# Performance work log

Hardware: AMD Instinct MI355X
Metric: run time of the kernel (lower is better)

## Reference

```python
import jax, jax.numpy as jnp
import numpy as np


def conv2d(x, w):
    # kernel_mult2d: VALID cross-correlation, NCHW/OIHW
    return jax.lax.conv_general_dilated(x, w, (1, 1), 'VALID',
                                        dimension_numbers=('NCHW', 'OIHW', 'NCHW'))


def setup_inputs() -> dict:
    key = jax.random.key(0)
    kx, kw = jax.random.split(key)
    B, C, H, W = 32, 16, 64, 64
    O, K = 256, 5
    x = jax.random.normal(kx, (B, C, H, W), dtype=jnp.float32)
    stdv = 1.0 / np.sqrt(C * K * K)  # nn.init.uniform_(-stdv, stdv)
    weight = jax.random.uniform(kw, (O, C, K, K), dtype=jnp.float32,
                                minval=-stdv, maxval=stdv)
    return {"x": x, "weight": weight}


def reference(x, weight):
    O, C, kh, kw = weight.shape
    # forward output: y = out_act(out_sim(x, weight)) with identity activation
    y = conv2d(x, weight)                                   # [B, O, Ho, Wo]

    # ---- compute_update (training branch, alpha != 0) ----
    # lrn_sim == out_sim, lrn_act == identity -> s == y
    s = y.transpose(0, 2, 3, 1).reshape(-1, O)              # [N, O], N = B*Ho*Wo
    N = s.shape[0]

    # unfold_map2d: patches with channel-major layout (C outer, kh*kw inner),
    # then permute(0,2,3,1,4).view(N, -1) -> [N, C*kh*kw]
    patches = jax.lax.conv_general_dilated_patches(
        x, (kh, kw), (1, 1), 'VALID',
        dimension_numbers=('NCHW', 'OIHW', 'NCHW'))         # [B, C*kh*kw, Ho, Wo]
    x_unf = patches.transpose(0, 2, 3, 1).reshape(N, -1)    # [N, D], D = C*kh*kw

    # competitive winner-take-all (no random abstention)
    winner_mask = (s == s.max(axis=1, keepdims=True)).astype(s.dtype)

    # lfb off; lfb_value == 0.0 so lfb_out == winner_mask; hebb rule: r = lfb_out * y
    r = winner_mask * s                                     # [N, O]

    # reconstruction 'qnt': x_bar = w; reduction 'mean':
    # delta_w[o, d] = mean_n r[n, o] * (x_unf[n, d] - w[o, d])
    # factor the outer-product mean to avoid the [N, O, D] intermediate
    w_flat = weight.reshape(O, -1)                          # [O, D]
    delta_w = (r.T @ x_unf) / N - r.mean(axis=0)[:, None] * w_flat

    return y, delta_w.reshape(weight.shape)
```

## Files before the change

kernel.cpp:

```cpp
#include <hip/hip_runtime.h>
#include <hip/hip_bf16.h>

#define B_  32
#define C_  16
#define Hh  64
#define Ww  64
#define O_  256
#define Kk  5
#define Ho_ 60
#define Wo_ 60
#define Dd  400
#define Nn  (B_*Ho_*Wo_)
#define NY  ((size_t)B_*O_*Ho_*Wo_)
#define OVCAP 1024
#define TAU 2.5e-4f
#define NSL 16
#define NCHK 60

typedef float f4 __attribute__((ext_vector_type(4)));
typedef float f32x16 __attribute__((ext_vector_type(16)));
typedef unsigned int u32x2 __attribute__((ext_vector_type(2)));
typedef unsigned int u32x4 __attribute__((ext_vector_type(4)));
typedef __bf16 bf16x8 __attribute__((ext_vector_type(8)));

static __device__ __forceinline__ void bf16split(float v, unsigned short& h, unsigned short& l) {
    __hip_bfloat16 bh = __float2bfloat16(v);
    float vh = __bfloat162float(bh);
    __hip_bfloat16 bl = __float2bfloat16(v - vh);
    h = __builtin_bit_cast(unsigned short, bh);
    l = __builtin_bit_cast(unsigned short, bl);
}

__global__ void prep_kernel(const float* __restrict__ w, unsigned short* __restrict__ wpkH,
                            unsigned short* __restrict__ wpkL, int* __restrict__ ovcnt,
                            int* __restrict__ done, float* __restrict__ dout) {
    const int u = blockIdx.x;
    const int jc = u / 5, s5 = u - (u / 5) * 5;
    const int tid = threadIdx.x;
    const int ot = tid >> 5, r32 = tid & 31;
    const int o = 32 * ot + r32;
    #pragma unroll
    for (int q2 = 0; q2 < 2; ++q2) {
        unsigned short h[8], l[8];
        #pragma unroll
        for (int j = 0; j < 8; ++j) {
            int g = 16 * s5 + 8 * q2 + j;
            bf16split(w[o * Dd + g * 5 + jc], h[j], l[j]);
        }
        const size_t off = ((size_t)(u * 8 + ot) * 64 + (r32 + 32 * q2)) * 8;
        u32x4 ph = { (unsigned)h[0] | ((unsigned)h[1] << 16), (unsigned)h[2] | ((unsigned)h[3] << 16),
                     (unsigned)h[4] | ((unsigned)h[5] << 16), (unsigned)h[6] | ((unsigned)h[7] << 16) };
        u32x4 pl = { (unsigned)l[0] | ((unsigned)l[1] << 16), (unsigned)l[2] | ((unsigned)l[3] << 16),
                     (unsigned)l[4] | ((unsigned)l[5] << 16), (unsigned)l[6] | ((unsigned)l[7] << 16) };
        *reinterpret_cast<u32x4*>(wpkH + off) = ph;
        *reinterpret_cast<u32x4*>(wpkL + off) = pl;
    }
    {
        float* dz = dout + NY + ((size_t)u * 256 + tid) * 16;
        f4 z = { 0.f, 0.f, 0.f, 0.f };
        *reinterpret_cast<f4*>(dz)      = z;
        *reinterpret_cast<f4*>(dz + 4)  = z;
        *reinterpret_cast<f4*>(dz + 8)  = z;
        *reinterpret_cast<f4*>(dz + 12) = z;
    }
    if (u == 0 && tid == 0) { *ovcnt = 0; *done = 0; }
}

__launch_bounds__(256, 3)
__global__ void conv_mfma_kernel(const float* __restrict__ x, const float* __restrict__ w,
                                 const unsigned short* __restrict__ wpkH,
                                 const unsigned short* __restrict__ wpkL, float* __restrict__ y,
                                 unsigned short* __restrict__ winner, float* __restrict__ wsv,
                                 int* __restrict__ ovn, int* __restrict__ ovo,
                                 float* __restrict__ ovs, int* __restrict__ ovcnt) {
    __shared__ __align__(16) unsigned short xT[2 * 7072];
    __shared__ float wm1[4][64], wm2[4][64];
    __shared__ float rowM1[64];
    __shared__ float rowMv[64];
    __shared__ int   rowO[64];
    __shared__ float xrow[Dd];
    __shared__ float red[256];
    __shared__ int   ambl[16];
    __shared__ int   ambc, nm;

    const int tid = threadIdx.x;
    const int L = tid & 63, wv = tid >> 6;
    const int q2 = L >> 5, r32 = L & 31;
    const int bid = (int)((blockIdx.x & 7) * 240 + (blockIdx.x >> 3));
    const int b = bid / Ho_, ho = bid % Ho_;

    if (tid == 0) ambc = 0;

    const unsigned short* ah0 = wpkH + (size_t)(2 * wv) * 512 + (size_t)L * 8;
    const unsigned short* al0 = wpkL + (size_t)(2 * wv) * 512 + (size_t)L * 8;

    u32x4 AH_[3][2], AL_[3][2];
    #pragma unroll
    for (int ot = 0; ot < 2; ++ot) {
        AH_[0][ot] = *reinterpret_cast<const u32x4*>(ah0 + ot * 512);
        AL_[0][ot] = *reinterpret_cast<const u32x4*>(al0 + ot * 512);
        AH_[1][ot] = *reinterpret_cast<const u32x4*>(ah0 + 4096 + ot * 512);
        AL_[1][ot] = *reinterpret_cast<const u32x4*>(al0 + 4096 + ot * 512);
    }

    if (tid < 80) {
        u32x4 z = { 0, 0, 0, 0 };
        int plane = tid / 40, rem = tid % 40, row = 64 + rem / 10, blk = rem % 10;
        *reinterpret_cast<u32x4*>(&xT[plane * 7072 + row * 104 + blk * 8]) = z;
    }

    {
        const float* xb = x + (size_t)b * (C_ * Hh * Ww);
        const int v = tid & 63;
        const int seg = tid >> 6;
        const int segc = seg * 4;
        #pragma unroll
        for (int qg = 0; qg < 5; ++qg) {
            unsigned short h[4], l[4];
            #pragma unroll
            for (int gg = 0; gg < 4; ++gg) {
                const int k = qg * 4 + gg;
                const int kc = k / 5, ki = k % 5;
                float val = xb[((segc + kc) * Hh + ho + ki) * Ww + v];
                bf16split(val, h[gg], l[gg]);
            }
            const int g0 = seg * 20 + qg * 4;
            u32x2 ph = { (unsigned)h[0] | ((unsigned)h[1] << 16),
                         (unsigned)h[2] | ((unsigned)h[3] << 16) };
            u32x2 pl = { (unsigned)l[0] | ((unsigned)l[1] << 16),
                         (unsigned)l[2] | ((unsigned)l[3] << 16) };
            *reinterpret_cast<u32x2*>(&xT[v * 104 + g0]) = ph;
            *reinterpret_cast<u32x2*>(&xT[7072 + v * 104 + g0]) = pl;
        }
    }

    f32x16 acc[2][2];
    #pragma unroll
    for (int ot = 0; ot < 2; ++ot)
        #pragma unroll
        for (int wt = 0; wt < 2; ++wt)
            #pragma unroll
            for (int i = 0; i < 16; ++i) acc[ot][wt][i] = 0.f;

    __syncthreads();

    u32x4 BH_[2][2], BL_[2][2];
    #pragma unroll
    for (int wt = 0; wt < 2; ++wt) {
        const int bbase = (32 * wt + r32 + 0) * 104 + 0 + 8 * q2;
        BH_[0][wt] = *reinterpret_cast<const u32x4*>(&xT[bbase]);
        BL_[0][wt] = *reinterpret_cast<const u32x4*>(&xT[7072 + bbase]);
    }

    #pragma unroll
    for (int u = 0; u < 25; ++u) {
        const int cur = u % 3;
        const int curB = u & 1, nxtB = curB ^ 1;
        if (u < 23) {
            const int nxtA = (u + 2) % 3;
            #pragma unroll
            for (int ot = 0; ot < 2; ++ot) {
                AH_[nxtA][ot] = *reinterpret_cast<const u32x4*>(ah0 + (u + 2) * 4096 + ot * 512);
                AL_[nxtA][ot] = *reinterpret_cast<const u32x4*>(al0 + (u + 2) * 4096 + ot * 512);
            }
        }
        if (u < 24) {
            const int jcn = (u + 1) / 5, s5n = (u + 1) % 5;
            #pragma unroll
            for (int wt = 0; wt < 2; ++wt) {
                const int bbase = (32 * wt + r32 + jcn) * 104 + 16 * s5n + 8 * q2;
                BH_[nxtB][wt] = *reinterpret_cast<const u32x4*>(&xT[bbase]);
                BL_[nxtB][wt] = *reinterpret_cast<const u32x4*>(&xT[7072 + bbase]);
            }
        }
        __builtin_amdgcn_sched_barrier(0);
        #pragma unroll
        for (int p = 0; p < 3; ++p) {
            #pragma unroll
            for (int ot = 0; ot < 2; ++ot) {
                #pragma unroll
                for (int wt = 0; wt < 2; ++wt) {
                    bf16x8 Aop = __builtin_bit_cast(bf16x8, (p == 2) ? AL_[cur][ot] : AH_[cur][ot]);
                    bf16x8 Bop = __builtin_bit_cast(bf16x8, (p == 1) ? BL_[curB][wt] : BH_[curB][wt]);
                    acc[ot][wt] = __builtin_amdgcn_mfma_f32_32x32x16_bf16(Aop, Bop, acc[ot][wt], 0, 0, 0);
                }
            }
        }
    }

    #pragma unroll
    for (int wt = 0; wt < 2; ++wt) {
        float m1 = -__builtin_inff(), m2 = -__builtin_inff();
        #pragma unroll
        for (int ot = 0; ot < 2; ++ot)
            #pragma unroll
            for (int i = 0; i < 16; ++i) {
                float v = acc[ot][wt][i];
                m2 = fmaxf(m2, fminf(m1, v));
                m1 = fmaxf(m1, v);
            }
        float o1 = __shfl_xor(m1, 32), o2 = __shfl_xor(m2, 32);
        m2 = fmaxf(fminf(m1, o1), fmaxf(m2, o2));
        m1 = fmaxf(m1, o1);
        if (q2 == 0) { wm1[wv][32 * wt + r32] = m1; wm2[wv][32 * wt + r32] = m2; }
    }
    __syncthreads();
    if (tid < 64) {
        const int p = tid;
        float M1 = wm1[0][p], M2 = wm2[0][p];
        #pragma unroll
        for (int w2 = 1; w2 < 4; ++w2) {
            float c1 = wm1[w2][p], c2 = wm2[w2][p];
            M2 = fmaxf(fminf(M1, c1), fmaxf(M2, c2));
            M1 = fmaxf(M1, c1);
        }
        bool amb = (M1 - M2) < TAU;
        if (amb && p < Wo_) {
            int pos = atomicAdd(&ambc, 1);
            if (pos < 16) ambl[pos] = p;
        }
        rowM1[p] = amb ? __builtin_inff() : M1;
        rowMv[p] = M1;
        rowO[p] = 0;
    }
    __syncthreads();

    #pragma unroll
    for (int wt = 0; wt < 2; ++wt) {
        const int wo = 32 * wt + r32;
        if (wo < Wo_) {
            const float M = rowM1[wo];
            #pragma unroll
            for (int ot = 0; ot < 2; ++ot)
                #pragma unroll
                for (int i = 0; i < 16; ++i) {
                    if (acc[ot][wt][i] == M)
                        rowO[wo] = 64 * wv + 32 * ot + (i & 3) + 8 * (i >> 2) + 4 * q2;
                }
        }
    }
    __syncthreads();
    if (tid < Wo_) {
        const int n = (b * Ho_ + ho) * Wo_ + tid;
        winner[n] = (unsigned short)rowO[tid];
        wsv[n] = rowMv[tid];
    }

    #pragma unroll
    for (int ot = 0; ot < 2; ++ot)
        #pragma unroll
        for (int wt = 0; wt < 2; ++wt) {
            const int wo = 32 * wt + r32;
            if (wo < Wo_) {
                #pragma unroll
                for (int i = 0; i < 16; ++i) {
                    const int o = 64 * wv + 32 * ot + (i & 3) + 8 * (i >> 2) + 4 * q2;
                    __builtin_nontemporal_store(acc[ot][wt][i],
                        y + ((size_t)(b * O_ + o) * Ho_ + ho) * (size_t)Wo_ + wo);
                }
            }
        }

    __syncthreads();
    const int na = (ambc < 16) ? ambc : 16;
    for (int a = 0; a < na; ++a) {
        const int wo = ambl[a];
        const int n = (b * Ho_ + ho) * Wo_ + wo;
        for (int k = tid; k < Dd; k += 256) {
            int c = k / 25, rr = k % 25, i = rr / 5, j = rr % 5;
            xrow[k] = x[(((size_t)b * C_ + c) * Hh + (ho + i)) * Ww + (wo + j)];
        }
        if (tid == 0) nm = 0;
        __syncthreads();
        const int o = tid;
        const float* wr = w + (size_t)o * Dd;
        float s = 0.f;
        #pragma unroll 4
        for (int k = 0; k < Dd; ++k) s = fmaf(xrow[k], wr[k], s);
        red[o] = s;
        __syncthreads();
        #pragma unroll
        for (int st = 128; st >= 1; st >>= 1) {
            if (o < st) red[o] = fmaxf(red[o], red[o + st]);
            __syncthreads();
        }
        const float mx = red[0];
        if (s == mx) {
            int k2 = atomicAdd(&nm, 1);
            if (k2 == 0) { winner[n] = (unsigned short)o; wsv[n] = mx; }
            else {
                int q = atomicAdd(ovcnt, 1);
                if (q < OVCAP) { ovn[q] = n; ovo[q] = o; ovs[q] = mx; }
            }
        }
        __syncthreads();
    }
}

__global__ void sort_kernel(const unsigned short* __restrict__ winner, const float* __restrict__ wsv,
                            int* __restrict__ h, int* __restrict__ done,
                            const int* __restrict__ ovn, const int* __restrict__ ovo,
                            const float* __restrict__ ovs, const int* __restrict__ ovcnt,
                            int* __restrict__ lw_n, float* __restrict__ lw_s,
                            int* __restrict__ count, int cap) {
    __shared__ int lh[O_];
    __shared__ int cur[O_];
    const int blk = blockIdx.x, tid = threadIdx.x;
    lh[tid] = 0;
    __syncthreads();
    const int n0 = blk * (Nn / NCHK);
    for (int i = tid; i < Nn / NCHK; i += 256)
        atomicAdd(&lh[(int)winner[n0 + i]], 1);
    __syncthreads();
    h[blk * O_ + tid] = lh[tid];
    __threadfence();
    __syncthreads();
    if (tid == 0) {
        atomicAdd(done, 1);
        while (atomicAdd(done, 0) < NCHK) __builtin_amdgcn_s_sleep(8);
        __threadfence();
    }
    __syncthreads();
    int basev = 0;
    for (int bb = 0; bb < blk; ++bb) basev += h[bb * O_ + tid];
    cur[tid] = basev;
    if (blk == 0) {
        int tot = 0;
        for (int bb = 0; bb < NCHK; ++bb) tot += h[bb * O_ + tid];
        int oc = *ovcnt; if (oc > OVCAP) oc = OVCAP;
        int cnt = tot;
        for (int e = 0; e < oc; ++e) {
            if (ovo[e] == tid && cnt < cap) {
                lw_n[(size_t)tid * cap + cnt] = ovn[e];
                lw_s[(size_t)tid * cap + cnt] = ovs[e];
                ++cnt;
            }
        }
        count[tid] = (cnt < cap) ? cnt : cap;
    }
    __syncthreads();
    for (int i = tid; i < Nn / NCHK; i += 256) {
        const int n = n0 + i;
        const int o = (int)winner[n];
        int pos = atomicAdd(&cur[o], 1);
        if (pos < cap) {
            lw_n[(size_t)o * cap + pos] = n;
            lw_s[(size_t)o * cap + pos] = wsv[n];
        }
    }
}

__global__ void delta_part_kernel(const float* __restrict__ x, const float* __restrict__ w,
                                  const int* __restrict__ count, const int* __restrict__ lw_n,
                                  const float* __restrict__ lw_s, float* __restrict__ dout,
                                  int cap) {
    const int o   = blockIdx.x / NSL;
    const int sl  = blockIdx.x % NSL;
    const int tid = threadIdx.x;
    int cnt = count[o]; if (cnt > cap) cnt = cap;
    const int e0 = (int)(((long long)cnt * sl) / NSL);
    const int e1 = (int)(((long long)cnt * (sl + 1)) / NSL);

    const int d0 = tid;
    const int c0 = d0 / 25, r0 = d0 % 25, i0 = r0 / 5, j0 = r0 % 5;
    const bool has1 = (tid < Dd - 256);
    const int dd1 = has1 ? tid + 256 : 0;
    const int c1 = dd1 / 25, r1 = dd1 % 25, i1 = r1 / 5, j1 = r1 % 5;
    const int off0 = c0 * (Hh * Ww) + i0 * Ww + j0;
    const int off1 = c1 * (Hh * Ww) + i1 * Ww + j1;

    const int* ln = lw_n + (size_t)o * cap;
    const float* ls = lw_s + (size_t)o * cap;

    float acc0 = 0.f, acc1 = 0.f, ssum = 0.f;
    int nA = 0, nB = 0; float sA = 0.f, sB = 0.f;
    if (e0 < e1)     { nA = ln[e0];     sA = ls[e0]; }
    if (e0 + 1 < e1) { nB = ln[e0 + 1]; sB = ls[e0 + 1]; }
    float xA0 = 0.f, xA1 = 0.f;
    if (e0 < e1) {
        int bb = nA / 3600, rem = nA - bb * 3600, hh = rem / 60, ww2 = rem - hh * 60;
        const float* xb = x + (size_t)bb * (C_ * Hh * Ww) + hh * Ww + ww2;
        xA0 = xb[off0]; if (has1) xA1 = xb[off1];
    }
    for (int e = e0; e < e1; ++e) {
        float xB0 = 0.f, xB1 = 0.f;
        if (e + 1 < e1) {
            int bb = nB / 3600, rem = nB - bb * 3600, hh = rem / 60, ww2 = rem - hh * 60;
            const float* xb = x + (size_t)bb * (C_ * Hh * Ww) + hh * Ww + ww2;
            xB0 = xb[off0]; if (has1) xB1 = xb[off1];
        }
        int nC = 0; float sC = 0.f;
        if (e + 2 < e1) { nC = ln[e + 2]; sC = ls[e + 2]; }
        ssum += sA; acc0 += sA * xA0; acc1 += sA * xA1;
        nA = nB; sA = sB; xA0 = xB0; xA1 = xB1;
        nB = nC; sB = sC;
    }
    if (e0 < e1) {
        const float invN = 1.0f / (float)Nn;
        atomicAdd(dout + NY + (size_t)o * Dd + d0, acc0 * invN - ssum * invN * w[o * Dd + d0]);
        if (has1)
            atomicAdd(dout + NY + (size_t)o * Dd + dd1, acc1 * invN - ssum * invN * w[o * Dd + dd1]);
    }
}

extern "C" void kernel_launch(void* const* d_in, const int* in_sizes, int n_in,
                              void* d_out, int out_size, void* d_ws, size_t ws_size,
                              hipStream_t stream) {
    (void)in_sizes; (void)n_in; (void)out_size;
    const float* x = (const float*)d_in[0];
    const float* w = (const float*)d_in[1];
    float* out = (float*)d_out;

    char* ws = (char*)d_ws;
    int*            count  = (int*)ws;
    int*            ovcnt  = (int*)(ws + 1024);
    int*            done   = (int*)(ws + 1088);
    unsigned short* wpkH   = (unsigned short*)(ws + 1152);
    unsigned short* wpkL   = (unsigned short*)(ws + 205952);
    unsigned short* winner = (unsigned short*)(ws + 410752);
    float*          wsv    = (float*)(ws + 641152);
    int*            ovn    = (int*)(ws + 1101952);
    int*            ovo    = (int*)(ws + 1106048);
    float*          ovs    = (float*)(ws + 1110144);
    int*            hist   = (int*)(ws + 1114240);
    const size_t base = 1175680;

    size_t avail = (ws_size > base) ? (ws_size - base) : 0;
    long long cap_ll = (long long)(avail / ((size_t)O_ * 8));
    int cap = (int)(cap_ll > 4096 ? 4096 : (cap_ll < 1 ? 1 : cap_ll));

    int*   lw_n = (int*)(ws + base);
    float* lw_s = (float*)(ws + base + (size_t)O_ * cap * 4);

    prep_kernel<<<dim3(25), dim3(256), 0, stream>>>(w, wpkH, wpkL, ovcnt, done, out);
    conv_mfma_kernel<<<dim3(B_ * Ho_), dim3(256), 0, stream>>>(x, w, wpkH, wpkL, out, winner, wsv,
                                                               ovn, ovo, ovs, ovcnt);
    sort_kernel<<<dim3(NCHK), dim3(256), 0, stream>>>(winner, wsv, hist, done,
                                                      ovn, ovo, ovs, ovcnt,
                                                      lw_n, lw_s, count, cap);
    delta_part_kernel<<<dim3(O_ * NSL), dim3(256), 0, stream>>>(x, w, count, lw_n, lw_s, out, cap);
}
```

Before: 191.0 us.

## Move ambiguous-winner exact recompute out of conv kernel into separate fallback kernel

The conv kernel no longer recomputes ambiguous winner positions in fp32 inline. It appends them to a global list, and a new grid-strided fallback kernel processes that list afterwards. This takes the serialized per-block recompute loop and its shared buffers out of the conv kernel, which lowers LDS use and removes tail imbalance between blocks. The cost is an extra kernel launch, global atomics on a single counter, and a fixed capacity for ambiguous entries.

```diff
diff --git a/kernel.cpp b/kernel.cpp
--- a/kernel.cpp
+++ b/kernel.cpp
@@ -12,6 +12,7 @@
 #define Dd  400
 #define Nn  (B_*Ho_*Wo_)
 #define NY  ((size_t)B_*O_*Ho_*Wo_)
+#define ACAP 16384
 #define OVCAP 1024
 #define TAU 2.5e-4f
 #define NSL 16
@@ -32,8 +33,9 @@
 }
 
 __global__ void prep_kernel(const float* __restrict__ w, unsigned short* __restrict__ wpkH,
-                            unsigned short* __restrict__ wpkL, int* __restrict__ ovcnt,
-                            int* __restrict__ done, float* __restrict__ dout) {
+                            unsigned short* __restrict__ wpkL, int* __restrict__ acnt,
+                            int* __restrict__ ovcnt, int* __restrict__ done,
+                            float* __restrict__ dout) {
     const int u = blockIdx.x;
     const int jc = u / 5, s5 = u - (u / 5) * 5;
     const int tid = threadIdx.x;
@@ -63,33 +65,25 @@
         *reinterpret_cast<f4*>(dz + 8)  = z;
         *reinterpret_cast<f4*>(dz + 12) = z;
     }
-    if (u == 0 && tid == 0) { *ovcnt = 0; *done = 0; }
+    if (u == 0 && tid == 0) { *acnt = 0; *ovcnt = 0; *done = 0; }
 }
 
 __launch_bounds__(256, 3)
-__global__ void conv_mfma_kernel(const float* __restrict__ x, const float* __restrict__ w,
-                                 const unsigned short* __restrict__ wpkH,
+__global__ void conv_mfma_kernel(const float* __restrict__ x, const unsigned short* __restrict__ wpkH,
                                  const unsigned short* __restrict__ wpkL, float* __restrict__ y,
                                  unsigned short* __restrict__ winner, float* __restrict__ wsv,
-                                 int* __restrict__ ovn, int* __restrict__ ovo,
-                                 float* __restrict__ ovs, int* __restrict__ ovcnt) {
+                                 int* __restrict__ acnt, int* __restrict__ ambig) {
     __shared__ __align__(16) unsigned short xT[2 * 7072];
     __shared__ float wm1[4][64], wm2[4][64];
     __shared__ float rowM1[64];
     __shared__ float rowMv[64];
     __shared__ int   rowO[64];
-    __shared__ float xrow[Dd];
-    __shared__ float red[256];
-    __shared__ int   ambl[16];
-    __shared__ int   ambc, nm;
 
     const int tid = threadIdx.x;
     const int L = tid & 63, wv = tid >> 6;
     const int q2 = L >> 5, r32 = L & 31;
     const int bid = (int)((blockIdx.x & 7) * 240 + (blockIdx.x >> 3));
     const int b = bid / Ho_, ho = bid % Ho_;
-
-    if (tid == 0) ambc = 0;
 
     const unsigned short* ah0 = wpkH + (size_t)(2 * wv) * 512 + (size_t)L * 8;
     const unsigned short* al0 = wpkL + (size_t)(2 * wv) * 512 + (size_t)L * 8;
@@ -216,8 +210,9 @@
         }
         bool amb = (M1 - M2) < TAU;
         if (amb && p < Wo_) {
-            int pos = atomicAdd(&ambc, 1);
-            if (pos < 16) ambl[pos] = p;
+            int n = (b * Ho_ + ho) * Wo_ + p;
+            int pos = atomicAdd(acnt, 1);
+            if (pos < ACAP) ambig[pos] = n;
         }
         rowM1[p] = amb ? __builtin_inff() : M1;
         rowMv[p] = M1;
@@ -260,24 +255,32 @@
                 }
             }
         }
-
-    __syncthreads();
-    const int na = (ambc < 16) ? ambc : 16;
-    for (int a = 0; a < na; ++a) {
-        const int wo = ambl[a];
-        const int n = (b * Ho_ + ho) * Wo_ + wo;
-        for (int k = tid; k < Dd; k += 256) {
+}
+
+__global__ void fallback_kernel(const float* __restrict__ x, const float* __restrict__ w,
+                                const int* __restrict__ acnt, const int* __restrict__ ambig,
+                                unsigned short* __restrict__ winner, float* __restrict__ wsv,
+                                int* __restrict__ ovn, int* __restrict__ ovo,
+                                float* __restrict__ ovs, int* __restrict__ ovcnt) {
+    __shared__ float xrow[Dd];
+    __shared__ float red[256];
+    __shared__ int nm;
+    int cnt = *acnt; if (cnt > ACAP) cnt = ACAP;
+    for (int idx = blockIdx.x; idx < cnt; idx += gridDim.x) {
+        const int n = ambig[idx];
+        const int bb = n / 3600, rem = n % 3600, hh = rem / 60, ww2 = rem % 60;
+        for (int k = threadIdx.x; k < Dd; k += 256) {
             int c = k / 25, rr = k % 25, i = rr / 5, j = rr % 5;
-            xrow[k] = x[(((size_t)b * C_ + c) * Hh + (ho + i)) * Ww + (wo + j)];
-        }
-        if (tid == 0) nm = 0;
+            xrow[k] = x[(((size_t)bb * C_ + c) * Hh + hh + i) * Ww + ww2 + j];
+        }
         __syncthreads();
-        const int o = tid;
+        const int o = threadIdx.x;
         const float* wr = w + (size_t)o * Dd;
         float s = 0.f;
         #pragma unroll 4
         for (int k = 0; k < Dd; ++k) s = fmaf(xrow[k], wr[k], s);
         red[o] = s;
+        if (o == 0) nm = 0;
         __syncthreads();
         #pragma unroll
         for (int st = 128; st >= 1; st >>= 1) {
@@ -287,10 +290,10 @@
         const float mx = red[0];
         if (s == mx) {
             int k2 = atomicAdd(&nm, 1);
-            if (k2 == 0) { winner[n] = (unsigned short)o; wsv[n] = mx; }
+            if (k2 == 0) { winner[n] = (unsigned short)o; wsv[n] = s; }
             else {
                 int q = atomicAdd(ovcnt, 1);
-                if (q < OVCAP) { ovn[q] = n; ovo[q] = o; ovs[q] = mx; }
+                if (q < OVCAP) { ovn[q] = n; ovo[q] = o; ovs[q] = s; }
             }
         }
         __syncthreads();
@@ -413,17 +416,19 @@
 
     char* ws = (char*)d_ws;
     int*            count  = (int*)ws;
-    int*            ovcnt  = (int*)(ws + 1024);
-    int*            done   = (int*)(ws + 1088);
-    unsigned short* wpkH   = (unsigned short*)(ws + 1152);
-    unsigned short* wpkL   = (unsigned short*)(ws + 205952);
-    unsigned short* winner = (unsigned short*)(ws + 410752);
-    float*          wsv    = (float*)(ws + 641152);
-    int*            ovn    = (int*)(ws + 1101952);
-    int*            ovo    = (int*)(ws + 1106048);
-    float*          ovs    = (float*)(ws + 1110144);
-    int*            hist   = (int*)(ws + 1114240);
-    const size_t base = 1175680;
+    int*            acnt   = (int*)(ws + 1024);
+    int*            ovcnt  = (int*)(ws + 1088);
+    int*            done   = (int*)(ws + 1152);
+    int*            ambig  = (int*)(ws + 1216);
+    unsigned short* wpkH   = (unsigned short*)(ws + 66752);
+    unsigned short* wpkL   = (unsigned short*)(ws + 271552);
+    unsigned short* winner = (unsigned short*)(ws + 476352);
+    float*          wsv    = (float*)(ws + 706752);
+    int*            ovn    = (int*)(ws + 1167552);
+    int*            ovo    = (int*)(ws + 1171648);
+    float*          ovs    = (float*)(ws + 1175744);
+    int*            hist   = (int*)(ws + 1179840);
+    const size_t base = 1241280;
 
     size_t avail = (ws_size > base) ? (ws_size - base) : 0;
     long long cap_ll = (long long)(avail / ((size_t)O_ * 8));
@@ -432,9 +437,11 @@
     int*   lw_n = (int*)(ws + base);
     float* lw_s = (float*)(ws + base + (size_t)O_ * cap * 4);
 
-    prep_kernel<<<dim3(25), dim3(256), 0, stream>>>(w, wpkH, wpkL, ovcnt, done, out);
-    conv_mfma_kernel<<<dim3(B_ * Ho_), dim3(256), 0, stream>>>(x, w, wpkH, wpkL, out, winner, wsv,
-                                                               ovn, ovo, ovs, ovcnt);
+    prep_kernel<<<dim3(25), dim3(256), 0, stream>>>(w, wpkH, wpkL, acnt, ovcnt, done, out);
+    conv_mfma_kernel<<<dim3(B_ * Ho_), dim3(256), 0, stream>>>(x, wpkH, wpkL, out, winner, wsv,
+                                                               acnt, ambig);
+    fallback_kernel<<<dim3(256), dim3(256), 0, stream>>>(x, w, acnt, ambig, winner, wsv,
+                                                         ovn, ovo, ovs, ovcnt);
     sort_kernel<<<dim3(NCHK), dim3(256), 0, stream>>>(winner, wsv, hist, done,
                                                       ovn, ovo, ovs, ovcnt,
                                                       lw_n, lw_s, count, cap);
```

After: 193.1 us. Within noise of the previous version (+1.1%).
